# Kernel tuning notes

Measured on AMD Instinct MI355X. Metric: run time of the kernel, lower is better.

Reference implementation:

```python
import math
import jax, jax.numpy as jnp
import numpy as np

# ---- matryoshka config (matches init_kwargs) ----
NUM_HEADS = 16
KV_GROUPS = 4
KV_REPEATS = NUM_HEADS // KV_GROUPS
QK_SIZES = [32, 64, 128]      # output_sizes // num_heads
HEAD_SIZES = [32, 64, 128]
D_MODEL = 2048
NEG_INF = -1e9


def _heads_reorder_indices(num_heads, sizes, reverse=False):
    parts = [[] for _ in range(num_heads)]
    offset, prev = 0, 0
    for size in sizes:
        seg = size - prev
        for h in range(num_heads):
            parts[h].append(np.arange(offset, offset + seg))
            offset += seg
        prev = size
    reorder = np.concatenate([a for head in parts for a in head])
    if reverse:
        rev = np.empty_like(reorder)
        rev[reorder] = np.arange(len(reorder))
        reorder = rev
    return jnp.asarray(reorder, dtype=jnp.int32)

Q_REORDER = _heads_reorder_indices(NUM_HEADS, QK_SIZES)
K_REORDER = _heads_reorder_indices(KV_GROUPS, QK_SIZES)
V_REORDER = _heads_reorder_indices(KV_GROUPS, HEAD_SIZES)
O_REORDER = _heads_reorder_indices(NUM_HEADS, HEAD_SIZES, reverse=True)


def setup_inputs() -> dict:
    key = jax.random.key(0)
    ks = jax.random.split(key, 9)
    B, S = 2, 1024
    dq = NUM_HEADS * QK_SIZES[-1]      # 2048
    dkv_q = KV_GROUPS * QK_SIZES[-1]   # 512
    dkv_v = KV_GROUPS * HEAD_SIZES[-1] # 512
    dout = NUM_HEADS * HEAD_SIZES[-1]  # 2048
    s = 0.02
    return {
        "x": jax.random.normal(ks[0], (B, S, D_MODEL), jnp.float32),
        "mask": jnp.tril(jnp.ones((S, S), jnp.bool_)),
        "Wq": jax.random.normal(ks[1], (D_MODEL, dq), jnp.float32) * s,
        "bq": jnp.zeros((dq,), jnp.float32),
        "Wk": jax.random.normal(ks[2], (D_MODEL, dkv_q), jnp.float32) * s,
        "bk": jnp.zeros((dkv_q,), jnp.float32),
        "Wv": jax.random.normal(ks[3], (D_MODEL, dkv_v), jnp.float32) * s,
        "bv": jnp.zeros((dkv_v,), jnp.float32),
        "Wo": jax.random.normal(ks[4], (dout, D_MODEL), jnp.float32) * s,
        "bo": jnp.zeros((D_MODEL,), jnp.float32),
    }


def reference(x, mask, Wq, bq, Wk, bk, Wv, bv, Wo, bo):
    B, S, _ = x.shape
    H, G, R = NUM_HEADS, KV_GROUPS, KV_REPEATS
    Dq, Dh = QK_SIZES[-1], HEAD_SIZES[-1]

    # matryoshka projections (full-size forward) + buffer-indexed reorder
    q = (x @ Wq + bq)[..., Q_REORDER]
    k = (x @ Wk + bk)[..., K_REORDER]
    v = (x @ Wv + bv)[..., V_REORDER]

    q = q.reshape(B, S, H, Dq).transpose(0, 2, 1, 3)   # [B,H,S,Dq]
    k = k.reshape(B, S, G, Dq).transpose(0, 2, 1, 3)   # [B,G,S,Dq]
    v = v.reshape(B, S, G, Dh).transpose(0, 2, 1, 3)   # [B,G,S,Dh]

    # GQA expansion: each group repeated kv_repeats times consecutively
    k = jnp.repeat(k, R, axis=1)  # [B,H,S,Dq]
    v = jnp.repeat(v, R, axis=1)  # [B,H,S,Dh]

    add_mask = jnp.where(mask, 0.0, NEG_INF).astype(x.dtype)  # [S,S]

    xs = []
    dp_cum = 0.0
    prev_qk, prev_hd = 0, 0
    for qk, hd in zip(QK_SIZES, HEAD_SIZES):
        # dot product over the NEW qk segment, accumulated over prefixes
        dp = jnp.einsum('bhqd,bhkd->bhqk', q[..., prev_qk:qk], k[..., prev_qk:qk])
        dp_cum = dp_cum + dp
        logits = dp_cum * (1.0 / math.sqrt(qk)) + add_mask
        attn = jax.nn.softmax(logits, axis=-1)
        # output only the NEW value segment for this nesting level
        xs.append(jnp.einsum('bhqk,bhkd->bhqd', attn, v[..., prev_hd:hd]))
        prev_qk, prev_hd = qk, hd

    out = jnp.concatenate(xs, axis=-1)                 # [B,H,S,Dh]
    out = out.transpose(0, 2, 1, 3).reshape(B, S, H * Dh)
    out = out[..., O_REORDER]
    return out @ Wo + bo
```

## Files before the change

### kernel.cpp

```cpp
#include <hip/hip_runtime.h>

typedef __attribute__((ext_vector_type(8))) __bf16 bf16x8;
typedef __attribute__((ext_vector_type(8))) unsigned short u16x8;
typedef __attribute__((ext_vector_type(4))) float f32x4;

#define XBOFF 0
#define WQKVOFF (XBOFF + 2048 * 2048)
#define WOOFF   (WQKVOFF + 3072 * 2048)
#define QOFF    (WOOFF + 2048 * 2048)
#define KOFF    (QOFF + 2048 * 2048)
#define VTOFF   (KOFF + 2048 * 512)
#define AOFF    (VTOFF + 2048 * 512)
__device__ ushort g_scratch[AOFF + 2048 * 2048];

__device__ __forceinline__ int nest_map(int n, int H) {
    int h = n >> 7, j = n & 127;
    if (j < 32) return h * 32 + j;
    if (j < 64) return H * 32 + h * 32 + (j - 32);
    return H * 64 + h * 64 + (j - 64);
}

__device__ __forceinline__ ushort f2bf(float f) {
    unsigned u = __builtin_bit_cast(unsigned, f);
    u += 0x7fffu + ((u >> 16) & 1u);
    return (ushort)(u >> 16);
}
__device__ __forceinline__ bf16x8 ld_frag(const ushort* p) {
    return __builtin_bit_cast(bf16x8, *(const u16x8*)p);
}
__device__ __forceinline__ void glds16(const ushort* g, ushort* s) {
    __builtin_amdgcn_global_load_lds(
        (const __attribute__((address_space(1))) void*)g,
        (__attribute__((address_space(3))) void*)s, 16, 0, 0);
}

__global__ __launch_bounds__(256) void prep_kernel(
    const float* __restrict__ x,
    const float* __restrict__ Wq, const float* __restrict__ Wk,
    const float* __restrict__ Wv, const float* __restrict__ Wo)
{
    const int bx = blockIdx.x;
    const int tid = threadIdx.x;

    if (bx < 2048) {
        size_t i = ((size_t)bx * 256 + tid) * 8;
        float4 f0 = *(const float4*)&x[i];
        float4 f1 = *(const float4*)&x[i + 4];
        union { uint4 v; ushort u[8]; } a;
        a.u[0] = f2bf(f0.x); a.u[1] = f2bf(f0.y); a.u[2] = f2bf(f0.z); a.u[3] = f2bf(f0.w);
        a.u[4] = f2bf(f1.x); a.u[5] = f2bf(f1.y); a.u[6] = f2bf(f1.z); a.u[7] = f2bf(f1.w);
        *(uint4*)&g_scratch[XBOFF + i] = a.v;
        return;
    }

    const float* W; int rowlen, H, mode, dstoff, t;
    if (bx < 3072)      { W = Wq; rowlen = 2048; H = 16; mode = 0; dstoff = WQKVOFF;               t = bx - 2048; }
    else if (bx < 3328) { W = Wk; rowlen = 512;  H = 4;  mode = 0; dstoff = WQKVOFF + 2048 * 2048; t = bx - 3072; }
    else if (bx < 3584) { W = Wv; rowlen = 512;  H = 4;  mode = 0; dstoff = WQKVOFF + 2560 * 2048; t = bx - 3328; }
    else                { W = Wo; rowlen = 2048; H = 16; mode = 1; dstoff = WOOFF;                 t = bx - 3584; }
    const int k0 = (t & 31) * 64;
    const int n0 = (t >> 5) * 64;

    __shared__ ushort T[64][66];
    const int r = tid >> 3, oct = tid & 7;

    #pragma unroll
    for (int rep = 0; rep < 2; ++rep) {
        int rr = r + rep * 32;
        int wrow = mode ? nest_map(k0 + rr, 16) : (k0 + rr);
        int wcol = mode ? (n0 + oct * 8) : nest_map(n0 + oct * 8, H);
        float4 f0 = *(const float4*)&W[(size_t)wrow * rowlen + wcol];
        float4 f1 = *(const float4*)&W[(size_t)wrow * rowlen + wcol + 4];
        ushort* d = &T[rr][oct * 8];
        d[0] = f2bf(f0.x); d[1] = f2bf(f0.y); d[2] = f2bf(f0.z); d[3] = f2bf(f0.w);
        d[4] = f2bf(f1.x); d[5] = f2bf(f1.y); d[6] = f2bf(f1.z); d[7] = f2bf(f1.w);
    }
    __syncthreads();
    #pragma unroll
    for (int rep = 0; rep < 2; ++rep) {
        int rr = r + rep * 32;
        union { uint4 v; ushort u[8]; } cv;
        #pragma unroll
        for (int i = 0; i < 8; ++i) cv.u[i] = T[oct * 8 + i][rr];
        *(uint4*)&g_scratch[dstoff + (size_t)(n0 + rr) * 2048 + k0 + oct * 8] = cv.v;
    }
}

__global__ __launch_bounds__(256) void gemm128_kernel(
    const float* __restrict__ b0, const float* __restrict__ b1,
    const float* __restrict__ b2, float* __restrict__ oext, int mode)
{
    __shared__ __align__(16) ushort SH[2 * 128 * 64];
    ushort* As = SH;
    ushort* Bs = SH + 128 * 64;
    const int n0 = blockIdx.x * 128;
    const int m0 = blockIdx.y * 128;
    const int tid = threadIdx.x;
    const int lane = tid & 63, wid = tid >> 6;
    const int wm = wid & 1, wn = wid >> 1;
    const int quad = lane >> 4, l16 = lane & 15;

    const ushort* A  = g_scratch + (mode ? AOFF : XBOFF);
    const ushort* Bt = g_scratch + (mode ? WOOFF : WQKVOFF);

    const bool vpath = (mode == 0) && (n0 >= 2560);
    const float* bias; ushort* outS = nullptr; int c0, oldim, H;
    if (mode == 1)      { bias = b0; c0 = n0; oldim = 2048; H = 0; }
    else if (n0 < 2048) { bias = b0; outS = g_scratch + QOFF; c0 = n0;        oldim = 2048; H = 16; }
    else if (n0 < 2560) { bias = b1; outS = g_scratch + KOFF; c0 = n0 - 2048; oldim = 512;  H = 4; }
    else                { bias = b2; outS = nullptr;          c0 = n0 - 2560; oldim = 512;  H = 4; }

    const int lrow = lane >> 3;
    const int lchunk = (lane & 7) ^ (lrow & 7);

    f32x4 acc[4][4];
    #pragma unroll
    for (int a = 0; a < 4; ++a)
        #pragma unroll
        for (int c = 0; c < 4; ++c) acc[a][c] = f32x4{0.f, 0.f, 0.f, 0.f};

    for (int kt = 0; kt < 32; ++kt) {
        const int k0 = kt * 64;
        #pragma unroll
        for (int it = 0; it < 4; ++it) {
            int rb = it * 32 + wid * 8;
            int r  = rb + lrow;
            glds16(&A[(size_t)(m0 + r) * 2048 + k0 + lchunk * 8], &As[rb * 64]);
            glds16(&Bt[(size_t)(n0 + r) * 2048 + k0 + lchunk * 8], &Bs[rb * 64]);
        }
        __syncthreads();
        #pragma unroll
        for (int kc = 0; kc < 2; ++kc) {
            bf16x8 af[4], bf[4];
            #pragma unroll
            for (int s = 0; s < 4; ++s) {
                int ra = wm * 64 + s * 16 + l16;
                int rbv = wn * 64 + s * 16 + l16;
                int ch = kc * 4 + quad;
                af[s] = ld_frag(&As[ra * 64 + ((ch ^ (ra & 7)) * 8)]);
                bf[s] = ld_frag(&Bs[rbv * 64 + ((ch ^ (rbv & 7)) * 8)]);
            }
            #pragma unroll
            for (int sm = 0; sm < 4; ++sm)
                #pragma unroll
                for (int sn = 0; sn < 4; ++sn)
                    acc[sm][sn] = __builtin_amdgcn_mfma_f32_16x16x32_bf16(
                        af[sm], bf[sn], acc[sm][sn], 0, 0, 0);
        }
        __syncthreads();
    }

    if (vpath) {
        #pragma unroll
        for (int sm = 0; sm < 4; ++sm)
        #pragma unroll
        for (int sn = 0; sn < 4; ++sn)
        #pragma unroll
        for (int i = 0; i < 4; ++i) {
            int r = wm * 64 + sm * 16 + quad * 4 + i;
            int loc = wn * 64 + sn * 16 + l16;
            float v = acc[sm][sn][i] + bias[nest_map(c0 + loc, 4)];
            SH[loc * 128 + (r ^ ((loc & 7) << 3))] = f2bf(v);
        }
        __syncthreads();
        const int dloc = tid >> 1, half = tid & 1;
        const int gg = c0 >> 7, bb = m0 >> 10, sb = m0 & 1023;
        ushort* vt = g_scratch + VTOFF;
        #pragma unroll
        for (int j = 0; j < 8; ++j) {
            int r = half * 64 + j * 8;
            uint4 v = *(uint4*)&SH[dloc * 128 + (r ^ ((dloc & 7) << 3))];
            *(uint4*)&vt[((size_t)((bb * 4 + gg) * 128 + dloc)) * 1024 + sb + r] = v;
        }
    } else {
        #pragma unroll
        for (int sm = 0; sm < 4; ++sm)
        #pragma unroll
        for (int sn = 0; sn < 4; ++sn)
        #pragma unroll
        for (int i = 0; i < 4; ++i) {
            int row = m0 + wm * 64 + sm * 16 + quad * 4 + i;
            int loc = wn * 64 + sn * 16 + l16;
            float v = acc[sm][sn][i];
            if (mode == 1) {
                oext[(size_t)row * 2048 + c0 + loc] = v + bias[c0 + loc];
            } else {
                v += bias[nest_map(c0 + loc, H)];
                outS[(size_t)row * oldim + c0 + loc] = f2bf(v);
            }
        }
    }
}

__global__ __launch_bounds__(256) void attn_kernel()
{
    const ushort* qb = g_scratch + QOFF;
    const ushort* kb = g_scratch + KOFF;
    const ushort* vt = g_scratch + VTOFF;
    ushort* att = g_scratch + AOFF;

    __shared__ ushort Ks[64][136];
    __shared__ ushort Vt[128][72];
    __shared__ ushort Ps[64][72];

    const int x = blockIdx.x, h = blockIdx.y, b = blockIdx.z;
    const int ks_half = x >> 1;
    const int qt = ((x ^ b) & 1) ? ks_half : 15 - ks_half;
    const int g = h >> 2;
    const int q0 = qt * 64;
    const int tid = threadIdx.x;
    const int lane = tid & 63, w = tid >> 6;
    const int quad = lane >> 4, l16 = lane & 15;

    bf16x8 qa[4];
    {
        const ushort* qrow =
            qb + ((size_t)((b * 1024 + q0 + w * 16 + l16) * 16 + h)) * 128;
        #pragma unroll
        for (int kc = 0; kc < 4; ++kc)
            qa[kc] = ld_frag(qrow + kc * 32 + quad * 8);
    }

    float m_s[3][4], l_s[3][4];
    #pragma unroll
    for (int l = 0; l < 3; ++l)
        #pragma unroll
        for (int i = 0; i < 4; ++i) { m_s[l][i] = -1e9f; l_s[l][i] = 0.0f; }
    f32x4 oacc[8];
    #pragma unroll
    for (int t2 = 0; t2 < 8; ++t2) oacc[t2] = f32x4{0.f, 0.f, 0.f, 0.f};
    const f32x4 fz = {0.f, 0.f, 0.f, 0.f};

    for (int kt = 0; kt <= qt; ++kt) {
        const int k0 = kt * 64;
        {
            int r16 = tid >> 4, oct16 = tid & 15;
            #pragma unroll
            for (int rep = 0; rep < 4; ++rep) {
                int row = r16 + rep * 16;
                *(uint4*)&Ks[row][oct16 * 8] =
                    *(const uint4*)&kb[(size_t)((b * 1024 + k0 + row) * 4 + g) * 128 + oct16 * 8];
            }
            int oct = tid & 7, dr = tid >> 3;
            #pragma unroll
            for (int rep = 0; rep < 4; ++rep) {
                int d = dr + rep * 32;
                *(uint4*)&Vt[d][oct * 8] =
                    *(const uint4*)&vt[((size_t)((b * 4 + g) * 128 + d)) * 1024 + k0 + oct * 8];
            }
        }
        __syncthreads();

        const bool diag = (kt == qt);

        f32x4 s0[4], s1[4], s2[4];
        #pragma unroll
        for (int n = 0; n < 4; ++n)
            s0[n] = __builtin_amdgcn_mfma_f32_16x16x32_bf16(
                qa[0], ld_frag(&Ks[n * 16 + l16][quad * 8]), fz, 0, 0, 0);
        #pragma unroll
        for (int n = 0; n < 4; ++n)
            s1[n] = __builtin_amdgcn_mfma_f32_16x16x32_bf16(
                qa[1], ld_frag(&Ks[n * 16 + l16][32 + quad * 8]), s0[n], 0, 0, 0);
        #pragma unroll
        for (int n = 0; n < 4; ++n)
            s2[n] = __builtin_amdgcn_mfma_f32_16x16x32_bf16(
                qa[2], ld_frag(&Ks[n * 16 + l16][64 + quad * 8]), s1[n], 0, 0, 0);
        #pragma unroll
        for (int n = 0; n < 4; ++n)
            s2[n] = __builtin_amdgcn_mfma_f32_16x16x32_bf16(
                qa[3], ld_frag(&Ks[n * 16 + l16][96 + quad * 8]), s2[n], 0, 0, 0);

        float sv[3][4][4], mx[3][4];
        #pragma unroll
        for (int l = 0; l < 3; ++l)
            #pragma unroll
            for (int i = 0; i < 4; ++i) mx[l][i] = -1e9f;
        #pragma unroll
        for (int n = 0; n < 4; ++n)
            #pragma unroll
            for (int i = 0; i < 4; ++i) {
                bool msk = diag &&
                    (k0 + n * 16 + l16 > q0 + w * 16 + quad * 4 + i);
                float x0 = msk ? -1e9f : s0[n][i] * 0.1767766953f;
                float x1 = msk ? -1e9f : s1[n][i] * 0.125f;
                float x2 = msk ? -1e9f : s2[n][i] * 0.0883883476f;
                sv[0][n][i] = x0; mx[0][i] = fmaxf(mx[0][i], x0);
                sv[1][n][i] = x1; mx[1][i] = fmaxf(mx[1][i], x1);
                sv[2][n][i] = x2; mx[2][i] = fmaxf(mx[2][i], x2);
            }
        #pragma unroll
        for (int d = 1; d < 16; d <<= 1)
            #pragma unroll
            for (int l = 0; l < 3; ++l)
                #pragma unroll
                for (int i = 0; i < 4; ++i)
                    mx[l][i] = fmaxf(mx[l][i], __shfl_xor(mx[l][i], d, 64));
        float al[3][4], rs[3][4];
        #pragma unroll
        for (int l = 0; l < 3; ++l)
            #pragma unroll
            for (int i = 0; i < 4; ++i) {
                float mn = fmaxf(m_s[l][i], mx[l][i]);
                al[l][i] = __expf(m_s[l][i] - mn);
                m_s[l][i] = mn;
                rs[l][i] = 0.f;
            }
        #pragma unroll
        for (int n = 0; n < 4; ++n)
            #pragma unroll
            for (int l = 0; l < 3; ++l)
                #pragma unroll
                for (int i = 0; i < 4; ++i) {
                    float p = __expf(sv[l][n][i] - m_s[l][i]);
                    sv[l][n][i] = p;
                    rs[l][i] += p;
                }
        #pragma unroll
        for (int d = 1; d < 16; d <<= 1)
            #pragma unroll
            for (int l = 0; l < 3; ++l)
                #pragma unroll
                for (int i = 0; i < 4; ++i)
                    rs[l][i] += __shfl_xor(rs[l][i], d, 64);
        #pragma unroll
        for (int l = 0; l < 3; ++l)
            #pragma unroll
            for (int i = 0; i < 4; ++i)
                l_s[l][i] = l_s[l][i] * al[l][i] + rs[l][i];
        #pragma unroll
        for (int t = 0; t < 8; ++t) {
            int lvl = (t < 2) ? 0 : (t < 4) ? 1 : 2;
            #pragma unroll
            for (int i = 0; i < 4; ++i) oacc[t][i] *= al[lvl][i];
        }

        const int obase[3] = {0, 2, 4}, onts[3] = {2, 2, 4}, voffs[3] = {0, 32, 64};
        #pragma unroll
        for (int l = 0; l < 3; ++l) {
            #pragma unroll
            for (int n = 0; n < 4; ++n)
                #pragma unroll
                for (int i = 0; i < 4; ++i)
                    Ps[w * 16 + quad * 4 + i][n * 16 + l16] = f2bf(sv[l][n][i]);
            #pragma unroll
            for (int kc = 0; kc < 2; ++kc) {
                bf16x8 pa = ld_frag(&Ps[w * 16 + l16][kc * 32 + quad * 8]);
                #pragma unroll
                for (int t = 0; t < 4; ++t) {
                    if (t < onts[l]) {
                        int vd = voffs[l] + t * 16 + l16;
                        bf16x8 vf = ld_frag(&Vt[vd][kc * 32 + quad * 8]);
                        oacc[obase[l] + t] = __builtin_amdgcn_mfma_f32_16x16x32_bf16(
                            pa, vf, oacc[obase[l] + t], 0, 0, 0);
                    }
                }
            }
        }
        __syncthreads();
    }

    float inv[3][4];
    #pragma unroll
    for (int l = 0; l < 3; ++l)
        #pragma unroll
        for (int i = 0; i < 4; ++i) {
            float L = l_s[l][i];
            inv[l][i] = (L > 0.f) ? (1.0f / L) : 0.f;
        }
    #pragma unroll
    for (int t = 0; t < 8; ++t) {
        int lvl = (t < 2) ? 0 : (t < 4) ? 1 : 2;
        #pragma unroll
        for (int i = 0; i < 4; ++i) {
            int srow = q0 + w * 16 + quad * 4 + i;
            att[(size_t)((b * 1024 + srow) * 16 + h) * 128 + t * 16 + l16] =
                f2bf(oacc[t][i] * inv[lvl][i]);
        }
    }
}

extern "C" void kernel_launch(void* const* d_in, const int* in_sizes, int n_in,
                              void* d_out, int out_size, void* d_ws, size_t ws_size,
                              hipStream_t stream)
{
    const float* x  = (const float*)d_in[0];
    const float* Wq = (const float*)d_in[2];
    const float* bq = (const float*)d_in[3];
    const float* Wk = (const float*)d_in[4];
    const float* bk = (const float*)d_in[5];
    const float* Wv = (const float*)d_in[6];
    const float* bv = (const float*)d_in[7];
    const float* Wo = (const float*)d_in[8];
    const float* bo = (const float*)d_in[9];
    float* out = (float*)d_out;
    (void)d_ws; (void)ws_size;

    dim3 blk(256, 1, 1);
    hipLaunchKernelGGL(prep_kernel, dim3(4608), blk, 0, stream, x, Wq, Wk, Wv, Wo);
    hipLaunchKernelGGL(gemm128_kernel, dim3(24, 16), blk, 0, stream,
                       bq, bk, bv, (float*)nullptr, 0);
    hipLaunchKernelGGL(attn_kernel, dim3(16, 16, 2), blk, 0, stream);
    hipLaunchKernelGGL(gemm128_kernel, dim3(16, 16), blk, 0, stream,
                       bo, nullptr, nullptr, out, 1);
}
```

Measured before the change: 294.2 us.

## Split attention KV range across two blocks with merge kernel, swizzle LDS

Each query tile's key range is now split between two blocks. Each block writes unnormalized fp32 partial outputs plus per-level max and sum to scratch, and a new merge kernel rescales the two halves and writes the bf16 attention output. This doubles grid parallelism and shortens the longest causal tiles, at the cost of an extra launch and roughly 40MB of fp32 partial traffic. LDS tiles for K, V^T and P also drop their padding in favor of an XOR swizzle to avoid bank conflicts.

Measured after the change: 329.7 us. 12.0% more time.

```diff
diff --git a/kernel.cpp b/kernel.cpp
--- a/kernel.cpp
+++ b/kernel.cpp
@@ -11,7 +11,9 @@
 #define KOFF    (QOFF + 2048 * 2048)
 #define VTOFF   (KOFF + 2048 * 512)
 #define AOFF    (VTOFF + 2048 * 512)
-__device__ ushort g_scratch[AOFF + 2048 * 2048];
+#define POOFF   (AOFF + 2048 * 2048)
+#define PMLOFF  (POOFF + 2 * 32768 * 128 * 2)
+__device__ __align__(16) ushort g_scratch[PMLOFF + 2 * 32768 * 6 * 2];
 
 __device__ __forceinline__ int nest_map(int n, int H) {
     int h = n >> 7, j = n & 127;
@@ -197,15 +199,17 @@
     const ushort* qb = g_scratch + QOFF;
     const ushort* kb = g_scratch + KOFF;
     const ushort* vt = g_scratch + VTOFF;
-    ushort* att = g_scratch + AOFF;
-
-    __shared__ ushort Ks[64][136];
-    __shared__ ushort Vt[128][72];
-    __shared__ ushort Ps[64][72];
+    float* PO  = (float*)(g_scratch + POOFF);
+    float* PML = (float*)(g_scratch + PMLOFF);
+
+    __shared__ __align__(16) ushort Ks[64 * 128];
+    __shared__ __align__(16) ushort Vt[128 * 64];
+    __shared__ __align__(16) ushort Ps[64 * 64];
 
     const int x = blockIdx.x, h = blockIdx.y, b = blockIdx.z;
-    const int ks_half = x >> 1;
-    const int qt = ((x ^ b) & 1) ? ks_half : 15 - ks_half;
+    const int qt = x >> 1, c = x & 1;
+    const int nk = qt + 1, half = nk >> 1;
+    const int lo = c ? half : 0, hi = c ? nk : half;
     const int g = h >> 2;
     const int q0 = qt * 64;
     const int tid = threadIdx.x;
@@ -231,21 +235,21 @@
     for (int t2 = 0; t2 < 8; ++t2) oacc[t2] = f32x4{0.f, 0.f, 0.f, 0.f};
     const f32x4 fz = {0.f, 0.f, 0.f, 0.f};
 
-    for (int kt = 0; kt <= qt; ++kt) {
+    for (int kt = lo; kt < hi; ++kt) {
         const int k0 = kt * 64;
         {
             int r16 = tid >> 4, oct16 = tid & 15;
             #pragma unroll
             for (int rep = 0; rep < 4; ++rep) {
                 int row = r16 + rep * 16;
-                *(uint4*)&Ks[row][oct16 * 8] =
+                *(uint4*)&Ks[row * 128 + ((oct16 ^ (row & 7)) * 8)] =
                     *(const uint4*)&kb[(size_t)((b * 1024 + k0 + row) * 4 + g) * 128 + oct16 * 8];
             }
             int oct = tid & 7, dr = tid >> 3;
             #pragma unroll
             for (int rep = 0; rep < 4; ++rep) {
                 int d = dr + rep * 32;
-                *(uint4*)&Vt[d][oct * 8] =
+                *(uint4*)&Vt[d * 64 + ((oct ^ (d & 7)) * 8)] =
                     *(const uint4*)&vt[((size_t)((b * 4 + g) * 128 + d)) * 1024 + k0 + oct * 8];
             }
         }
@@ -255,21 +259,29 @@
 
         f32x4 s0[4], s1[4], s2[4];
         #pragma unroll
-        for (int n = 0; n < 4; ++n)
+        for (int n = 0; n < 4; ++n) {
+            int r = n * 16 + l16;
             s0[n] = __builtin_amdgcn_mfma_f32_16x16x32_bf16(
-                qa[0], ld_frag(&Ks[n * 16 + l16][quad * 8]), fz, 0, 0, 0);
-        #pragma unroll
-        for (int n = 0; n < 4; ++n)
+                qa[0], ld_frag(&Ks[r * 128 + (((0 + quad) ^ (r & 7)) * 8)]), fz, 0, 0, 0);
+        }
+        #pragma unroll
+        for (int n = 0; n < 4; ++n) {
+            int r = n * 16 + l16;
             s1[n] = __builtin_amdgcn_mfma_f32_16x16x32_bf16(
-                qa[1], ld_frag(&Ks[n * 16 + l16][32 + quad * 8]), s0[n], 0, 0, 0);
-        #pragma unroll
-        for (int n = 0; n < 4; ++n)
+                qa[1], ld_frag(&Ks[r * 128 + (((4 + quad) ^ (r & 7)) * 8)]), s0[n], 0, 0, 0);
+        }
+        #pragma unroll
+        for (int n = 0; n < 4; ++n) {
+            int r = n * 16 + l16;
             s2[n] = __builtin_amdgcn_mfma_f32_16x16x32_bf16(
-                qa[2], ld_frag(&Ks[n * 16 + l16][64 + quad * 8]), s1[n], 0, 0, 0);
-        #pragma unroll
-        for (int n = 0; n < 4; ++n)
+                qa[2], ld_frag(&Ks[r * 128 + (((8 + quad) ^ (r & 7)) * 8)]), s1[n], 0, 0, 0);
+        }
+        #pragma unroll
+        for (int n = 0; n < 4; ++n) {
+            int r = n * 16 + l16;
             s2[n] = __builtin_amdgcn_mfma_f32_16x16x32_bf16(
-                qa[3], ld_frag(&Ks[n * 16 + l16][96 + quad * 8]), s2[n], 0, 0, 0);
+                qa[3], ld_frag(&Ks[r * 128 + (((12 + quad) ^ (r & 7)) * 8)]), s2[n], 0, 0, 0);
+        }
 
         float sv[3][4][4], mx[3][4];
         #pragma unroll
@@ -341,16 +353,21 @@
             #pragma unroll
             for (int n = 0; n < 4; ++n)
                 #pragma unroll
-                for (int i = 0; i < 4; ++i)
-                    Ps[w * 16 + quad * 4 + i][n * 16 + l16] = f2bf(sv[l][n][i]);
+                for (int i = 0; i < 4; ++i) {
+                    int prow = w * 16 + quad * 4 + i;
+                    int col = n * 16 + l16;
+                    Ps[prow * 64 + ((((col >> 3) ^ (prow & 7)) << 3) | (col & 7))] =
+                        f2bf(sv[l][n][i]);
+                }
             #pragma unroll
             for (int kc = 0; kc < 2; ++kc) {
-                bf16x8 pa = ld_frag(&Ps[w * 16 + l16][kc * 32 + quad * 8]);
+                int prow = w * 16 + l16;
+                bf16x8 pa = ld_frag(&Ps[prow * 64 + (((kc * 4 + quad) ^ (prow & 7)) * 8)]);
                 #pragma unroll
                 for (int t = 0; t < 4; ++t) {
                     if (t < onts[l]) {
                         int vd = voffs[l] + t * 16 + l16;
-                        bf16x8 vf = ld_frag(&Vt[vd][kc * 32 + quad * 8]);
+                        bf16x8 vf = ld_frag(&Vt[vd * 64 + (((kc * 4 + quad) ^ (vd & 7)) * 8)]);
                         oacc[obase[l] + t] = __builtin_amdgcn_mfma_f32_16x16x32_bf16(
                             pa, vf, oacc[obase[l] + t], 0, 0, 0);
                     }
@@ -360,24 +377,68 @@
         __syncthreads();
     }
 
-    float inv[3][4];
-    #pragma unroll
-    for (int l = 0; l < 3; ++l)
-        #pragma unroll
-        for (int i = 0; i < 4; ++i) {
-            float L = l_s[l][i];
-            inv[l][i] = (L > 0.f) ? (1.0f / L) : 0.f;
-        }
+    const size_t rowbase = ((size_t)(c * 2 + b) * 16 + h) * 1024;
     #pragma unroll
     for (int t = 0; t < 8; ++t) {
-        int lvl = (t < 2) ? 0 : (t < 4) ? 1 : 2;
         #pragma unroll
         for (int i = 0; i < 4; ++i) {
             int srow = q0 + w * 16 + quad * 4 + i;
-            att[(size_t)((b * 1024 + srow) * 16 + h) * 128 + t * 16 + l16] =
-                f2bf(oacc[t][i] * inv[lvl][i]);
-        }
-    }
+            PO[(rowbase + srow) * 128 + t * 16 + l16] = oacc[t][i];
+        }
+    }
+    #pragma unroll
+    for (int lvl = 0; lvl < 3; ++lvl) {
+        if ((l16 >> 1) == lvl && l16 < 6) {
+            bool isl = (l16 & 1);
+            #pragma unroll
+            for (int i = 0; i < 4; ++i) {
+                int srow = q0 + w * 16 + quad * 4 + i;
+                PML[(rowbase + srow) * 6 + l16] = isl ? l_s[lvl][i] : m_s[lvl][i];
+            }
+        }
+    }
+}
+
+__global__ __launch_bounds__(256) void merge_kernel()
+{
+    const float* PO  = (const float*)(g_scratch + POOFF);
+    const float* PML = (const float*)(g_scratch + PMLOFF);
+    ushort* att = g_scratch + AOFF;
+
+    const int idx = blockIdx.x * 256 + threadIdx.x;
+    const int R = idx >> 4;
+    const int seg = idx & 15;
+    const int lvl = (seg < 4) ? 0 : (seg < 8) ? 1 : 2;
+    const int NR = 32768;
+
+    float m0 = PML[(size_t)(0 * NR + R) * 6 + 2 * lvl];
+    float l0 = PML[(size_t)(0 * NR + R) * 6 + 2 * lvl + 1];
+    float m1 = PML[(size_t)(1 * NR + R) * 6 + 2 * lvl];
+    float l1 = PML[(size_t)(1 * NR + R) * 6 + 2 * lvl + 1];
+    float M = fmaxf(m0, m1);
+    float w0 = __expf(m0 - M), w1 = __expf(m1 - M);
+    float den = w0 * l0 + w1 * l1;
+    float inv = (den > 0.f) ? (1.0f / den) : 0.f;
+    w0 *= inv; w1 *= inv;
+
+    const int d0 = seg * 8;
+    float4 a0 = *(const float4*)&PO[((size_t)(0 * NR + R)) * 128 + d0];
+    float4 a1 = *(const float4*)&PO[((size_t)(0 * NR + R)) * 128 + d0 + 4];
+    float4 c0 = *(const float4*)&PO[((size_t)(1 * NR + R)) * 128 + d0];
+    float4 c1 = *(const float4*)&PO[((size_t)(1 * NR + R)) * 128 + d0 + 4];
+
+    union { uint4 v; ushort u[8]; } o;
+    o.u[0] = f2bf(w0 * a0.x + w1 * c0.x);
+    o.u[1] = f2bf(w0 * a0.y + w1 * c0.y);
+    o.u[2] = f2bf(w0 * a0.z + w1 * c0.z);
+    o.u[3] = f2bf(w0 * a0.w + w1 * c0.w);
+    o.u[4] = f2bf(w0 * a1.x + w1 * c1.x);
+    o.u[5] = f2bf(w0 * a1.y + w1 * c1.y);
+    o.u[6] = f2bf(w0 * a1.z + w1 * c1.z);
+    o.u[7] = f2bf(w0 * a1.w + w1 * c1.w);
+
+    const int b = R >> 14, h = (R >> 10) & 15, s = R & 1023;
+    *(uint4*)&att[((size_t)((b * 1024 + s) * 16 + h)) * 128 + d0] = o.v;
 }
 
 extern "C" void kernel_launch(void* const* d_in, const int* in_sizes, int n_in,
@@ -400,7 +461,8 @@
     hipLaunchKernelGGL(prep_kernel, dim3(4608), blk, 0, stream, x, Wq, Wk, Wv, Wo);
     hipLaunchKernelGGL(gemm128_kernel, dim3(24, 16), blk, 0, stream,
                        bq, bk, bv, (float*)nullptr, 0);
-    hipLaunchKernelGGL(attn_kernel, dim3(16, 16, 2), blk, 0, stream);
+    hipLaunchKernelGGL(attn_kernel, dim3(32, 16, 2), blk, 0, stream);
+    hipLaunchKernelGGL(merge_kernel, dim3(2048), blk, 0, stream);
     hipLaunchKernelGGL(gemm128_kernel, dim3(16, 16), blk, 0, stream,
                        bo, nullptr, nullptr, out, 1);
 }
```
